# Performance work log

Hardware: AMD Instinct MI355X
Metric: run time of the kernel (lower is better)

## Reference

```python
import jax, jax.numpy as jnp
import numpy as np

SPARSITY = 0.05
D_MODEL, HIDDEN = 1024, 64
B, S = 4, 4096

def setup_inputs() -> dict:
    key = jax.random.key(0)
    k1, k2, k3 = jax.random.split(key, 3)
    embeddings = jax.random.normal(k1, (B, S, D_MODEL), dtype=jnp.float32)
    # Kaiming-ish scaled params for the importance MLP
    W1 = jax.random.normal(k2, (D_MODEL, HIDDEN), dtype=jnp.float32) / np.sqrt(D_MODEL)
    b1 = jnp.zeros((HIDDEN,), dtype=jnp.float32)
    W2 = jax.random.normal(k3, (HIDDEN, 1), dtype=jnp.float32) / np.sqrt(HIDDEN)
    b2 = jnp.zeros((1,), dtype=jnp.float32)
    return {"embeddings": embeddings, "W1": W1, "b1": b1, "W2": W2, "b2": b2}

def reference(embeddings, W1, b1, W2, b2):
    batch_size, seq_len, _ = embeddings.shape
    k = max(1, int(seq_len * SPARSITY))
    # importance MLP -> scores [B, S]
    h = jax.nn.relu(jnp.einsum('bsd,dh->bsh', embeddings, W1) + b1)
    scores = (jnp.einsum('bsh,ho->bso', h, W2) + b2)[..., 0]
    _, top_indices = jax.lax.top_k(scores, k)  # [B, k]
    # Each row i of attention_pattern[b] has 1/k at columns top_indices[b].
    # Build [B, S] column mask once, broadcast over the query dim.
    col_mask = jnp.zeros((batch_size, seq_len), dtype=embeddings.dtype)
    col_mask = col_mask.at[jnp.arange(batch_size)[:, None], top_indices].set(1.0 / k)
    attention_pattern = jnp.broadcast_to(col_mask[:, None, :], (batch_size, seq_len, seq_len))
    return attention_pattern, top_indices
```

## Files before the change

kernel.cpp:

```cpp
#include <hip/hip_runtime.h>

#define BB 4
#define SS 4096
#define DM 1024
#define HID 64
#define KTOP 204
static constexpr size_t PATTERN_N = (size_t)BB * SS * SS;

typedef float f4 __attribute__((ext_vector_type(4)));
typedef float f32x4 __attribute__((ext_vector_type(4)));
typedef _Float16 h8v __attribute__((ext_vector_type(8)));

#define SCORES_OFF 0
#define WHF_OFF 16384
#define WLF_OFF 49152

__global__ __launch_bounds__(256) void k0_wconv(
    const float* __restrict__ W1, _Float16* __restrict__ whf,
    _Float16* __restrict__ wlf) {
  const int gid = blockIdx.x * 256 + threadIdx.x;
  const int l = gid & 63;
  const int nt = (gid >> 6) & 3;
  const int k0 = gid >> 8;
  const int kb = k0 * 32 + (l >> 4) * 8;
  const int n = nt * 16 + (l & 15);
  h8v hi, lo;
#pragma unroll
  for (int j = 0; j < 8; ++j) {
    float w = W1[(size_t)(kb + j) * HID + n] * 1024.f;
    _Float16 h = (_Float16)w;
    hi[j] = h;
    lo[j] = (_Float16)((w - (float)h) * 4096.f);
  }
  reinterpret_cast<h8v*>(whf)[(k0 * 4 + nt) * 64 + l] = hi;
  reinterpret_cast<h8v*>(wlf)[(k0 * 4 + nt) * 64 + l] = lo;
}

__global__ __launch_bounds__(256) void k1_mfma(
    const float* __restrict__ emb, const _Float16* __restrict__ whf,
    const _Float16* __restrict__ wlf, const float* __restrict__ b1,
    const float* __restrict__ W2, const float* __restrict__ b2,
    float* __restrict__ scores) {
  const int tid = threadIdx.x;
  const int l = tid & 63;
  const int wv = tid >> 6;
  const int tokw = blockIdx.x * 128 + wv * 32;
  const int lrow = l & 15;
  const int lk8 = (l >> 4) * 8;

  const float* __restrict__ ap0 = emb + (size_t)(tokw + lrow) * DM + lk8;
  const float* __restrict__ ap1 = emb + (size_t)(tokw + 16 + lrow) * DM + lk8;
  const h8v* __restrict__ bhp = reinterpret_cast<const h8v*>(whf);
  const h8v* __restrict__ blp = reinterpret_cast<const h8v*>(wlf);

  f32x4 acc0[2][4], acc1[2][4];
#pragma unroll
  for (int mt = 0; mt < 2; ++mt)
#pragma unroll
    for (int nt = 0; nt < 4; ++nt) {
      acc0[mt][nt] = (f32x4){0.f, 0.f, 0.f, 0.f};
      acc1[mt][nt] = (f32x4){0.f, 0.f, 0.f, 0.f};
    }

  f4 a0c, a1c, a0c2, a1c2;
  h8v bhc[4], blc[4];
  a0c = *reinterpret_cast<const f4*>(ap0);
  a0c2 = *reinterpret_cast<const f4*>(ap0 + 4);
  a1c = *reinterpret_cast<const f4*>(ap1);
  a1c2 = *reinterpret_cast<const f4*>(ap1 + 4);
#pragma unroll
  for (int nt = 0; nt < 4; ++nt) {
    bhc[nt] = bhp[nt * 64 + l];
    blc[nt] = blp[nt * 64 + l];
  }

#pragma unroll 2
  for (int k0 = 0; k0 < 32; ++k0) {
    f4 a0n, a1n, a0n2, a1n2;
    h8v bhn[4], bln[4];
    if (k0 < 31) {
      const int koff = (k0 + 1) * 32;
      a0n = *reinterpret_cast<const f4*>(ap0 + koff);
      a0n2 = *reinterpret_cast<const f4*>(ap0 + koff + 4);
      a1n = *reinterpret_cast<const f4*>(ap1 + koff);
      a1n2 = *reinterpret_cast<const f4*>(ap1 + koff + 4);
#pragma unroll
      for (int nt = 0; nt < 4; ++nt) {
        bhn[nt] = bhp[((k0 + 1) * 4 + nt) * 64 + l];
        bln[nt] = blp[((k0 + 1) * 4 + nt) * 64 + l];
      }
    }
    h8v ah[2], al[2];
#pragma unroll
    for (int j = 0; j < 4; ++j) {
      _Float16 h;
      h = (_Float16)a0c[j];  ah[0][j] = h;
      al[0][j] = (_Float16)((a0c[j] - (float)h) * 4096.f);
      h = (_Float16)a0c2[j]; ah[0][4 + j] = h;
      al[0][4 + j] = (_Float16)((a0c2[j] - (float)h) * 4096.f);
      h = (_Float16)a1c[j];  ah[1][j] = h;
      al[1][j] = (_Float16)((a1c[j] - (float)h) * 4096.f);
      h = (_Float16)a1c2[j]; ah[1][4 + j] = h;
      al[1][4 + j] = (_Float16)((a1c2[j] - (float)h) * 4096.f);
    }
#pragma unroll
    for (int mt = 0; mt < 2; ++mt)
#pragma unroll
      for (int nt = 0; nt < 4; ++nt) {
        acc0[mt][nt] = __builtin_amdgcn_mfma_f32_16x16x32_f16(
            ah[mt], bhc[nt], acc0[mt][nt], 0, 0, 0);
        acc1[mt][nt] = __builtin_amdgcn_mfma_f32_16x16x32_f16(
            al[mt], bhc[nt], acc1[mt][nt], 0, 0, 0);
        acc1[mt][nt] = __builtin_amdgcn_mfma_f32_16x16x32_f16(
            ah[mt], blc[nt], acc1[mt][nt], 0, 0, 0);
      }
    if (k0 < 31) {
      a0c = a0n; a0c2 = a0n2; a1c = a1n; a1c2 = a1n2;
#pragma unroll
      for (int nt = 0; nt < 4; ++nt) { bhc[nt] = bhn[nt]; blc[nt] = bln[nt]; }
    }
  }

  float w2v[4], b1v[4];
#pragma unroll
  for (int nt = 0; nt < 4; ++nt) {
    w2v[nt] = W2[nt * 16 + lrow];
    b1v[nt] = b1[nt * 16 + lrow];
  }
  const float bb2 = b2[0];
#pragma unroll
  for (int mt = 0; mt < 2; ++mt)
#pragma unroll
    for (int i = 0; i < 4; ++i) {
      float p = 0.f;
#pragma unroll
      for (int nt = 0; nt < 4; ++nt) {
        float hs = (acc0[mt][nt][i] + 0x1p-12f * acc1[mt][nt][i]) * 0x1p-10f +
                   b1v[nt];
        hs = hs > 0.f ? hs : 0.f;
        p = fmaf(hs, w2v[nt], p);
      }
      p += __shfl_xor(p, 1, 64);
      p += __shfl_xor(p, 2, 64);
      p += __shfl_xor(p, 4, 64);
      p += __shfl_xor(p, 8, 64);
      if (lrow == 0)
        scores[tokw + mt * 16 + (l >> 4) * 4 + i] = p + bb2;
    }
}

__global__ __launch_bounds__(256) void k2_topk(
    const float* __restrict__ scores, float* __restrict__ out_idx) {
  __shared__ __align__(16) float sc[SS];
  __shared__ int red[256];
  const int tid = threadIdx.x;
  const int b = blockIdx.x >> 6;
  const int ic = blockIdx.x & 63;
  const float* row = scores + (size_t)b * SS;
#pragma unroll
  for (int q = 0; q < 4; ++q) {
    int f = tid + q * 256;
    *reinterpret_cast<f4*>(&sc[f * 4]) =
        *reinterpret_cast<const f4*>(&row[f * 4]);
  }
  __syncthreads();
  const int il = tid & 63;
  const int part = tid >> 6;
  const int i = ic * 64 + il;
  const float si = sc[i];
  const f4* s4 = reinterpret_cast<const f4*>(sc);
  int cnt = 0;
  for (int j4 = part * 256; j4 < part * 256 + 256; ++j4) {
    f4 v = s4[j4];
    int j = j4 * 4;
    cnt += (int)(v.x > si) + (int)((v.x == si) & (j + 0 < i));
    cnt += (int)(v.y > si) + (int)((v.y == si) & (j + 1 < i));
    cnt += (int)(v.z > si) + (int)((v.z == si) & (j + 2 < i));
    cnt += (int)(v.w > si) + (int)((v.w == si) & (j + 3 < i));
  }
  red[tid] = cnt;
  __syncthreads();
  if (tid < 64) {
    int tot = red[tid] + red[tid + 64] + red[tid + 128] + red[tid + 192];
    if (tot < KTOP) out_idx[b * KTOP + tot] = (float)(ic * 64 + tid);
  }
}

__global__ __launch_bounds__(256) void k3_pattern(
    const float* __restrict__ out_idx, float* __restrict__ pat) {
  __shared__ __align__(16) float mask[SS];
  const int tid = threadIdx.x;
  const int b  = blockIdx.x >> 8;
  const int r0 = (blockIdx.x & 255) * 16;
  const f4 zero = (f4){0.f, 0.f, 0.f, 0.f};
#pragma unroll
  for (int q = 0; q < 4; ++q) {
    int f = tid + q * 256;
    *reinterpret_cast<f4*>(&mask[f * 4]) = zero;
  }
  __syncthreads();
  if (tid < KTOP) {
    int c = (int)out_idx[b * KTOP + tid];
    mask[c] = 1.0f / (float)KTOP;
  }
  __syncthreads();
  const f4 m0 = *reinterpret_cast<const f4*>(&mask[(tid)*4]);
  const f4 m1 = *reinterpret_cast<const f4*>(&mask[(tid + 256) * 4]);
  const f4 m2 = *reinterpret_cast<const f4*>(&mask[(tid + 512) * 4]);
  const f4 m3 = *reinterpret_cast<const f4*>(&mask[(tid + 768) * 4]);
  for (int r = 0; r < 16; ++r) {
    f4* p4 = reinterpret_cast<f4*>(pat + ((size_t)b * SS + r0 + r) * SS);
    __builtin_nontemporal_store(m0, &p4[tid]);
    __builtin_nontemporal_store(m1, &p4[tid + 256]);
    __builtin_nontemporal_store(m2, &p4[tid + 512]);
    __builtin_nontemporal_store(m3, &p4[tid + 768]);
  }
}

extern "C" void kernel_launch(void* const* d_in, const int* in_sizes, int n_in,
                              void* d_out, int out_size, void* d_ws,
                              size_t ws_size, hipStream_t stream) {
  const float* emb = (const float*)d_in[0];
  const float* W1  = (const float*)d_in[1];
  const float* b1  = (const float*)d_in[2];
  const float* W2  = (const float*)d_in[3];
  const float* b2  = (const float*)d_in[4];
  float* out = (float*)d_out;
  float* pat     = out;
  float* out_idx = out + PATTERN_N;
  float* scores = out + SCORES_OFF;
  _Float16* whf = (_Float16*)(out + WHF_OFF);
  _Float16* wlf = (_Float16*)(out + WLF_OFF);

  k0_wconv<<<dim3(32), dim3(256), 0, stream>>>(W1, whf, wlf);
  k1_mfma<<<dim3((BB * SS) / 128), dim3(256), 0, stream>>>(emb, whf, wlf, b1,
                                                           W2, b2, scores);
  k2_topk<<<dim3(BB * (SS / 64)), dim3(256), 0, stream>>>(scores, out_idx);
  k3_pattern<<<dim3((BB * SS) / 16), dim3(256), 0, stream>>>(out_idx, pat);
}
```

Measured before the change: 121.5 us.

## Use packed 64-bit sortable keys in top-k rank, shrink pattern rows, plain stores

```diff
diff --git a/kernel.cpp b/kernel.cpp
--- a/kernel.cpp
+++ b/kernel.cpp
@@ -10,6 +10,7 @@
 typedef float f4 __attribute__((ext_vector_type(4)));
 typedef float f32x4 __attribute__((ext_vector_type(4)));
 typedef _Float16 h8v __attribute__((ext_vector_type(8)));
+typedef unsigned long long ull2 __attribute__((ext_vector_type(2)));
 
 #define SCORES_OFF 0
 #define WHF_OFF 16384
@@ -149,39 +150,39 @@
     }
 }
 
-__global__ __launch_bounds__(256) void k2_topk(
+__global__ __launch_bounds__(512) void k2_topk(
     const float* __restrict__ scores, float* __restrict__ out_idx) {
-  __shared__ __align__(16) float sc[SS];
-  __shared__ int red[256];
+  __shared__ __align__(16) unsigned long long ku[SS];
+  __shared__ int red[512];
   const int tid = threadIdx.x;
   const int b = blockIdx.x >> 6;
   const int ic = blockIdx.x & 63;
   const float* row = scores + (size_t)b * SS;
 #pragma unroll
-  for (int q = 0; q < 4; ++q) {
-    int f = tid + q * 256;
-    *reinterpret_cast<f4*>(&sc[f * 4]) =
-        *reinterpret_cast<const f4*>(&row[f * 4]);
+  for (int q = 0; q < 8; ++q) {
+    const int j = tid + q * 512;
+    unsigned u = __builtin_bit_cast(unsigned, row[j]);
+    u ^= (unsigned)((int)u >> 31) | 0x80000000u;
+    ku[j] = ((unsigned long long)u << 32) | (unsigned)(SS - 1 - j);
   }
   __syncthreads();
   const int il = tid & 63;
   const int part = tid >> 6;
   const int i = ic * 64 + il;
-  const float si = sc[i];
-  const f4* s4 = reinterpret_cast<const f4*>(sc);
+  const unsigned long long ki = ku[i];
+  const ull2* kp = reinterpret_cast<const ull2*>(ku);
   int cnt = 0;
-  for (int j4 = part * 256; j4 < part * 256 + 256; ++j4) {
-    f4 v = s4[j4];
-    int j = j4 * 4;
-    cnt += (int)(v.x > si) + (int)((v.x == si) & (j + 0 < i));
-    cnt += (int)(v.y > si) + (int)((v.y == si) & (j + 1 < i));
-    cnt += (int)(v.z > si) + (int)((v.z == si) & (j + 2 < i));
-    cnt += (int)(v.w > si) + (int)((v.w == si) & (j + 3 < i));
+#pragma unroll 8
+  for (int m = part * 256; m < part * 256 + 256; ++m) {
+    ull2 v = kp[m];
+    cnt += (int)(v.x > ki) + (int)(v.y > ki);
   }
   red[tid] = cnt;
   __syncthreads();
   if (tid < 64) {
-    int tot = red[tid] + red[tid + 64] + red[tid + 128] + red[tid + 192];
+    int tot = 0;
+#pragma unroll
+    for (int p = 0; p < 8; ++p) tot += red[tid + p * 64];
     if (tot < KTOP) out_idx[b * KTOP + tot] = (float)(ic * 64 + tid);
   }
 }
@@ -190,8 +191,8 @@
     const float* __restrict__ out_idx, float* __restrict__ pat) {
   __shared__ __align__(16) float mask[SS];
   const int tid = threadIdx.x;
-  const int b  = blockIdx.x >> 8;
-  const int r0 = (blockIdx.x & 255) * 16;
+  const int b  = blockIdx.x >> 9;
+  const int r0 = (blockIdx.x & 511) * 8;
   const f4 zero = (f4){0.f, 0.f, 0.f, 0.f};
 #pragma unroll
   for (int q = 0; q < 4; ++q) {
@@ -208,12 +209,12 @@
   const f4 m1 = *reinterpret_cast<const f4*>(&mask[(tid + 256) * 4]);
   const f4 m2 = *reinterpret_cast<const f4*>(&mask[(tid + 512) * 4]);
   const f4 m3 = *reinterpret_cast<const f4*>(&mask[(tid + 768) * 4]);
-  for (int r = 0; r < 16; ++r) {
+  for (int r = 0; r < 8; ++r) {
     f4* p4 = reinterpret_cast<f4*>(pat + ((size_t)b * SS + r0 + r) * SS);
-    __builtin_nontemporal_store(m0, &p4[tid]);
-    __builtin_nontemporal_store(m1, &p4[tid + 256]);
-    __builtin_nontemporal_store(m2, &p4[tid + 512]);
-    __builtin_nontemporal_store(m3, &p4[tid + 768]);
+    p4[tid]       = m0;
+    p4[tid + 256] = m1;
+    p4[tid + 512] = m2;
+    p4[tid + 768] = m3;
   }
 }
 
@@ -235,6 +236,6 @@
   k0_wconv<<<dim3(32), dim3(256), 0, stream>>>(W1, whf, wlf);
   k1_mfma<<<dim3((BB * SS) / 128), dim3(256), 0, stream>>>(emb, whf, wlf, b1,
                                                            W2, b2, scores);
-  k2_topk<<<dim3(BB * (SS / 64)), dim3(256), 0, stream>>>(scores, out_idx);
-  k3_pattern<<<dim3((BB * SS) / 16), dim3(256), 0, stream>>>(out_idx, pat);
-}
+  k2_topk<<<dim3(BB * 64), dim3(512), 0, stream>>>(scores, out_idx);
+  k3_pattern<<<dim3((BB * SS) / 8), dim3(256), 0, stream>>>(out_idx, pat);
+}
```

New measurement: 104.2 us. 14.2% less time.
